# Kernel tuning notes

Hardware: AMD Instinct MI355X
Metric: run time of the kernel (lower is better)

Reference implementation:

```python
import jax, jax.numpy as jnp
import numpy as np

B, S, D, H = 4, 1024, 512, 8
DH = D // H  # dim_head = 64
LN_EPS = 1e-5
COS_EPS = 1e-8


def setup_inputs() -> dict:
    key = jax.random.key(0)
    ks = jax.random.split(key, 8)
    q = jax.random.normal(ks[0], (B, S, D), dtype=jnp.float32)
    k = jax.random.normal(ks[1], (B, S, D), dtype=jnp.float32)
    v = jax.random.normal(ks[2], (B, S, D), dtype=jnp.float32)
    ln_g = jnp.ones((D,), jnp.float32)
    ln_b = jnp.zeros((D,), jnp.float32)
    W_in = jax.random.normal(ks[3], (D, D), dtype=jnp.float32) / np.sqrt(D)
    W_out = jax.random.normal(ks[4], (D, D), dtype=jnp.float32) / np.sqrt(D)
    b_out = jnp.zeros((D,), jnp.float32)
    cov_w = jnp.float32(0.6)
    var_w = jnp.float32(0.2)
    return {"q": q, "k": k, "v": v, "ln_g": ln_g, "ln_b": ln_b,
            "W_in": W_in, "W_out": W_out, "b_out": b_out,
            "cov_w": cov_w, "var_w": var_w}


def reference(q, k, v, ln_g, ln_b, W_in, W_out, b_out, cov_w, var_w):
    def transform(x):
        # input_layernorm followed by bias-free input_linear
        mu = jnp.mean(x, axis=-1, keepdims=True)
        var = jnp.var(x, axis=-1, keepdims=True)
        xn = (x - mu) * jax.lax.rsqrt(var + LN_EPS) * ln_g + ln_b
        y = xn @ W_in
        # 'q n (h d) -> h q n d'
        return y.reshape(B, S, H, DH).transpose(2, 0, 1, 3)

    f_q = transform(q)  # [h, b, n, d]
    f_k = transform(k)  # [h, b, m, d]
    f_v = transform(v)  # [h, b, m, d]

    # cosine_distance(f_q, f_k^T)
    dots = jnp.einsum('hbnd,hbmd->hbnm', f_q, f_k)
    qn = jnp.linalg.norm(f_q, axis=-1)  # [h, b, n]
    kn = jnp.linalg.norm(f_k, axis=-1)  # [h, b, m]
    cosine_sim = dots / (qn[..., :, None] * kn[..., None, :] + COS_EPS)

    # basic_attention_components
    q_c = f_q - jnp.mean(f_q, axis=-1, keepdims=True)
    k_c = f_k - jnp.mean(f_k, axis=-1, keepdims=True)
    cov_component = jnp.einsum('hbnd,hbmd->hbnm', q_c, k_c) / DH
    q_var = jnp.var(f_q, axis=-1, ddof=1)  # torch.var unbiased=True
    k_var = jnp.var(f_k, axis=-1, ddof=1)
    var_component = (q_var[..., :, None] * k_var[..., None, :]) / DH

    # fixed learned-scalar mixing (dynamic_weight=False path)
    attn = (cov_w * cov_component + var_w * var_component
            + (1.0 - cov_w - var_w) * cosine_sim)

    out = jnp.einsum('hbnm,hbmd->hbnd', attn, f_v)
    # 'h q n d -> q n (h d)'
    out = out.transpose(1, 2, 0, 3).reshape(B, S, D)
    return out @ W_out + b_out
```

## Files before the change

### kernel.cpp

```cpp
#include <hip/hip_runtime.h>


#define R_TOT 4096
#define DD 512
#define HB_N 32

typedef __attribute__((ext_vector_type(8))) short short8;
typedef __attribute__((ext_vector_type(4))) float f32x4;

static __device__ inline unsigned short f2bf(float f) {
    union { float f; unsigned u; } x{f};
    unsigned r = x.u + 0x7fff + ((x.u >> 16) & 1);
    return (unsigned short)(r >> 16);
}

static __device__ inline unsigned scale2(unsigned u, float a, float b) {
    float lo = __uint_as_float(u << 16);
    float hi = __uint_as_float(u & 0xffff0000u);
    return (unsigned)f2bf(lo * a) | ((unsigned)f2bf(hi * b) << 16);
}

static __device__ inline void async_cp16(const unsigned short* g, unsigned short* l) {
    __builtin_amdgcn_global_load_lds(
        (const __attribute__((address_space(1))) unsigned int*)g,
        (__attribute__((address_space(3))) unsigned int*)l, 16, 0, 0);
}

__global__ __launch_bounds__(256) void k1_ln_prep(
    const float* __restrict__ q, const float* __restrict__ k, const float* __restrict__ v,
    const float* __restrict__ ln_g, const float* __restrict__ ln_b,
    const float* __restrict__ Win, const float* __restrict__ Wout,
    unsigned short* __restrict__ xn, unsigned short* __restrict__ WinT,
    unsigned short* __restrict__ WoutT)
{
    int blk = blockIdx.x;
    int t = threadIdx.x, lane = t & 63, wv = t >> 6;
    if (blk < 3072) {
        int row = blk * 4 + wv;
        const float* src = (row < R_TOT) ? q : (row < 2 * R_TOT ? k : v);
        const float* x = src + (size_t)(row & (R_TOT - 1)) * DD + lane * 8;
        float4 v0 = *(const float4*)x;
        float4 v1 = *(const float4*)(x + 4);
        float s  = v0.x + v0.y + v0.z + v0.w + v1.x + v1.y + v1.z + v1.w;
        float s2 = v0.x * v0.x + v0.y * v0.y + v0.z * v0.z + v0.w * v0.w
                 + v1.x * v1.x + v1.y * v1.y + v1.z * v1.z + v1.w * v1.w;
        #pragma unroll
        for (int o = 32; o; o >>= 1) { s += __shfl_xor(s, o); s2 += __shfl_xor(s2, o); }
        float mu = s * (1.f / 512.f);
        float var = s2 * (1.f / 512.f) - mu * mu;
        float rstd = rsqrtf(var + 1e-5f);
        float4 g0 = *(const float4*)(ln_g + lane * 8);
        float4 g1 = *(const float4*)(ln_g + lane * 8 + 4);
        float4 b0 = *(const float4*)(ln_b + lane * 8);
        float4 b1 = *(const float4*)(ln_b + lane * 8 + 4);
        float e0 = (v0.x - mu) * rstd * g0.x + b0.x;
        float e1 = (v0.y - mu) * rstd * g0.y + b0.y;
        float e2 = (v0.z - mu) * rstd * g0.z + b0.z;
        float e3 = (v0.w - mu) * rstd * g0.w + b0.w;
        float e4 = (v1.x - mu) * rstd * g1.x + b1.x;
        float e5 = (v1.y - mu) * rstd * g1.y + b1.y;
        float e6 = (v1.z - mu) * rstd * g1.z + b1.z;
        float e7 = (v1.w - mu) * rstd * g1.w + b1.w;
        uint4 o;
        o.x = (unsigned)f2bf(e0) | ((unsigned)f2bf(e1) << 16);
        o.y = (unsigned)f2bf(e2) | ((unsigned)f2bf(e3) << 16);
        o.z = (unsigned)f2bf(e4) | ((unsigned)f2bf(e5) << 16);
        o.w = (unsigned)f2bf(e6) | ((unsigned)f2bf(e7) << 16);
        *(uint4*)(xn + (size_t)row * DD + lane * 8) = o;
    } else {
        __shared__ float tl[64][65];
        int bb = blk - 3072;
        const float* src = (bb & 64) ? Wout : Win;
        unsigned short* dst = (bb & 64) ? WoutT : WinT;
        int tile = bb & 63;
        int r0 = (tile >> 3) * 64, c0 = (tile & 7) * 64;
        #pragma unroll
        for (int rep = 0; rep < 16; rep++) {
            int rr = rep * 4 + (t >> 6), cc = t & 63;
            tl[rr][cc] = src[(size_t)(r0 + rr) * DD + c0 + cc];
        }
        __syncthreads();
        #pragma unroll
        for (int rep = 0; rep < 16; rep++) {
            int rr = rep * 4 + (t >> 6), cc = t & 63;
            dst[(size_t)(c0 + rr) * DD + r0 + cc] = f2bf(tl[cc][rr]);
        }
    }
}

__global__ __launch_bounds__(256) void gemm_qkv(
    const unsigned short* __restrict__ A, const unsigned short* __restrict__ Bt,
    unsigned short* __restrict__ A2, unsigned short* __restrict__ Kt,
    unsigned short* __restrict__ Vt, float* __restrict__ kinv,
    float* __restrict__ kvar, float* __restrict__ kmu)
{
    __shared__ __align__(16) char smbuf[39936];
    unsigned short* AsF = (unsigned short*)smbuf;
    unsigned short* BsF = (unsigned short*)(smbuf + 16384);
    int t = threadIdx.x, lane = t & 63, wv = t >> 6;
    int quad = lane >> 4, l15 = lane & 15;
    int m0 = blockIdx.y * 128, n0 = blockIdx.x * 128;
    int wr = (wv >> 1) * 64, wc = (wv & 1) * 64;
    int swz = l15 & 7;
    int r8 = lane >> 3, cc8 = lane & 7;
    f32x4 acc[4][4] = {};
    for (int kt = 0; kt < 512; kt += 64) {
        __syncthreads();
        #pragma unroll
        for (int gi = 0; gi < 4; gi++) {
            int grp = wv * 4 + gi;
            int row = grp * 8 + r8;
            int col = kt + ((cc8 ^ (row & 7)) << 3);
            async_cp16(A + (size_t)(m0 + row) * 512 + col, AsF + grp * 512);
            async_cp16(Bt + (size_t)(n0 + row) * 512 + col, BsF + grp * 512);
        }
        __syncthreads();
        #pragma unroll
        for (int kk = 0; kk < 2; kk++) {
            short8 af[4], bf[4];
            int ksl = ((kk * 4 + quad) ^ swz) << 3;
            #pragma unroll
            for (int i = 0; i < 4; i++) af[i] = *(const short8*)&AsF[(wr + i * 16 + l15) * 64 + ksl];
            #pragma unroll
            for (int j = 0; j < 4; j++) bf[j] = *(const short8*)&BsF[(wc + j * 16 + l15) * 64 + ksl];
            #pragma unroll
            for (int i = 0; i < 4; i++)
                #pragma unroll
                for (int j = 0; j < 4; j++)
                    acc[i][j] = __builtin_amdgcn_mfma_f32_16x16x32_bf16(af[i], bf[j], acc[i][j], 0, 0, 0);
        }
    }
    __syncthreads();

    unsigned short* tile = (unsigned short*)(smbuf + wv * 9216);
    float* st     = (float*)(smbuf + 36864 + wv * 768);
    float* st_inv = st;
    float* st_var = st + 64;
    float* st_mu  = st + 128;

    int typ  = m0 >> 12;
    int rloc = (m0 & 4095) + wr;
    int b = rloc >> 10, sb = rloc & 1023;
    int h = (n0 + wc) >> 6;
    int hb = h * 4 + b;

    if (typ < 2) {
        #pragma unroll
        for (int i = 0; i < 4; i++)
            #pragma unroll
            for (int r = 0; r < 4; r++) {
                float a0 = acc[i][0][r], a1 = acc[i][1][r], a2 = acc[i][2][r], a3 = acc[i][3][r];
                float s1 = a0 + a1 + a2 + a3;
                float s2 = a0 * a0 + a1 * a1 + a2 * a2 + a3 * a3;
                #pragma unroll
                for (int o = 1; o < 16; o <<= 1) { s1 += __shfl_xor(s1, o); s2 += __shfl_xor(s2, o); }
                if (l15 == 0) {
                    int sl = i * 16 + quad * 4 + r;
                    float mu = s1 * (1.f / 64.f);
                    st_inv[sl] = rsqrtf(fmaxf(s2, 1e-20f));
                    st_var[sl] = (s2 - 64.f * mu * mu) * (1.f / 63.f);
                    st_mu[sl]  = mu;
                }
            }
    }
    #pragma unroll
    for (int i = 0; i < 4; i++)
        #pragma unroll
        for (int j = 0; j < 4; j++)
            #pragma unroll
            for (int r = 0; r < 4; r++) {
                int sl = i * 16 + quad * 4 + r, d = j * 16 + l15;
                unsigned short bv = f2bf(acc[i][j][r]);
                tile[(typ == 0) ? (sl * 72 + d) : (d * 72 + sl)] = bv;
            }

    if (typ == 0) {
        unsigned short* ob = A2 + ((size_t)hb * 1024 + sb) * 160;
        #pragma unroll
        for (int it = 0; it < 8; it++) {
            int sl = it * 8 + (lane >> 3), ch = (lane & 7) * 8;
            uint4 raw = *(uint4*)&tile[sl * 72 + ch];
            *(uint4*)(ob + (size_t)sl * 160 + ch) = raw;
            float iv = st_inv[sl];
            uint4 o2;
            o2.x = scale2(raw.x, iv, iv); o2.y = scale2(raw.y, iv, iv);
            o2.z = scale2(raw.z, iv, iv); o2.w = scale2(raw.w, iv, iv);
            *(uint4*)(ob + (size_t)sl * 160 + 64 + ch) = o2;
        }
        {
            int sl = lane;
            uint4 z = {0, 0, 0, 0};
            uint4 t0 = z;
            t0.x = (unsigned)f2bf(st_var[sl]) | ((unsigned)f2bf(st_mu[sl]) << 16);
            unsigned short* p = ob + (size_t)sl * 160 + 128;
            *(uint4*)p = t0;
            *(uint4*)(p + 8) = z; *(uint4*)(p + 16) = z; *(uint4*)(p + 24) = z;
        }
    } else if (typ == 1) {
        unsigned short* kb = Kt + (size_t)hb * 64 * 1024 + sb;
        #pragma unroll
        for (int it = 0; it < 8; it++) {
            int d = it * 8 + (lane >> 3), ch = (lane & 7) * 8;
            uint4 raw = *(uint4*)&tile[d * 72 + ch];
            *(uint4*)(kb + (size_t)d * 1024 + ch) = raw;
        }
        int mi = hb * 1024 + sb + lane;
        kinv[mi] = st_inv[lane];
        kvar[mi] = st_var[lane];
        kmu[mi]  = st_mu[lane];
    } else {
        unsigned short* vb = Vt + (size_t)hb * 64 * 1024 + sb;
        #pragma unroll
        for (int it = 0; it < 8; it++) {
            int d = it * 8 + (lane >> 3), ch = (lane & 7) * 8;
            uint4 raw = *(uint4*)&tile[d * 72 + ch];
            *(uint4*)(vb + (size_t)d * 1024 + ch) = raw;
        }
    }
}

__global__ __launch_bounds__(256) void k45_ktv(
    const unsigned short* __restrict__ Kt, const unsigned short* __restrict__ Vt,
    const float* __restrict__ kinv, const float* __restrict__ kvar,
    const float* __restrict__ kmu, unsigned short* __restrict__ B2t,
    const float* __restrict__ covp, const float* __restrict__ varp)
{
    __shared__ __align__(16) unsigned short As[144][136];
    __shared__ __align__(16) unsigned short Bs[64][136];
    __shared__ float sinv[128], svar[128], smu[128];
    int hb = blockIdx.x;
    int t = threadIdx.x, lane = t & 63, wv = t >> 6;
    int quad = lane >> 4, l15 = lane & 15;
    float cov = covp[0], vw = varp[0];
    float c1 = cov * (1.f / 64.f), cw = 1.f - cov - vw;
    float vw64 = vw * (1.f / 64.f), c2 = -cov;
    const unsigned short* Kb = Kt + (size_t)hb * 64 * 1024;
    const unsigned short* Vb = Vt + (size_t)hb * 64 * 1024;
    int sbase = hb * 1024;
    if (t < 224) {
        int row = 130 + (t >> 4), co = (t & 15) * 8;
        uint4 z = {0, 0, 0, 0};
        *(uint4*)&As[row][co] = z;
    }
    f32x4 acc[9] = {};
    for (int kc = 0; kc < 8; kc++) {
        __syncthreads();
        if (t < 128) {
            int m = kc * 128 + t;
            sinv[t] = kinv[sbase + m]; svar[t] = kvar[sbase + m]; smu[t] = kmu[sbase + m];
        }
        uint4 kraw[4];
        #pragma unroll
        for (int i = 0; i < 4; i++) {
            int id = i * 256 + t, row = id >> 4, co = (id & 15) * 8;
            kraw[i] = *(const uint4*)(Kb + (size_t)row * 1024 + kc * 128 + co);
            *(uint4*)&As[row][co] = kraw[i];
            uint4 vr = *(const uint4*)(Vb + (size_t)row * 1024 + kc * 128 + co);
            *(uint4*)&Bs[row][co] = vr;
        }
        __syncthreads();
        #pragma unroll
        for (int i = 0; i < 4; i++) {
            int id = i * 256 + t, row = id >> 4, co = (id & 15) * 8;
            float4 iva = *(const float4*)&sinv[co];
            float4 ivb = *(const float4*)&sinv[co + 4];
            uint4 o;
            o.x = scale2(kraw[i].x, iva.x, iva.y); o.y = scale2(kraw[i].y, iva.z, iva.w);
            o.z = scale2(kraw[i].z, ivb.x, ivb.y); o.w = scale2(kraw[i].w, ivb.z, ivb.w);
            *(uint4*)&As[64 + row][co] = o;
        }
        if (t < 32) {
            int which = t >> 4, j0 = (t & 15) * 8;
            const float* sp = (which ? smu : svar) + j0;
            uint4 o;
            o.x = (unsigned)f2bf(sp[0]) | ((unsigned)f2bf(sp[1]) << 16);
            o.y = (unsigned)f2bf(sp[2]) | ((unsigned)f2bf(sp[3]) << 16);
            o.z = (unsigned)f2bf(sp[4]) | ((unsigned)f2bf(sp[5]) << 16);
            o.w = (unsigned)f2bf(sp[6]) | ((unsigned)f2bf(sp[7]) << 16);
            *(uint4*)&As[128 + which][j0] = o;
        }
        __syncthreads();
        #pragma unroll
        for (int kk = 0; kk < 4; kk++) {
            short8 bfrag = *(const short8*)&Bs[wv * 16 + l15][kk * 32 + quad * 8];
            #pragma unroll
            for (int mt = 0; mt < 9; mt++) {
                short8 afrag = *(const short8*)&As[mt * 16 + l15][kk * 32 + quad * 8];
                acc[mt] = __builtin_amdgcn_mfma_f32_16x16x32_bf16(afrag, bfrag, acc[mt], 0, 0, 0);
            }
        }
    }
    unsigned short* ob = B2t + (size_t)hb * 10240;
    int d = wv * 16 + l15;
    #pragma unroll
    for (int mt = 0; mt < 9; mt++)
        #pragma unroll
        for (int r = 0; r < 4; r++) {
            int kk = mt * 16 + quad * 4 + r;
            float scale = (kk < 64) ? c1 : (kk < 128) ? cw : (kk == 128) ? vw64 : (kk == 129) ? c2 : 0.f;
            ob[d * 160 + kk] = f2bf(scale * acc[mt][r]);
        }
}

__global__ __launch_bounds__(256) void k6_apply(
    const unsigned short* __restrict__ A2, const unsigned short* __restrict__ B2t,
    unsigned short* __restrict__ g)
{
    int hb = blockIdx.y, h = hb >> 2, b = hb & 3;
    int m0 = blockIdx.x * 128;
    int t = threadIdx.x, lane = t & 63, wv = t >> 6;
    int quad = lane >> 4, l15 = lane & 15;
    __shared__ __align__(16) unsigned short As[128][40];
    __shared__ __align__(16) unsigned short Bs[64][40];
    const unsigned short* Ab = A2 + (size_t)hb * 1024 * 160;
    const unsigned short* Bb = B2t + (size_t)hb * 10240;
    f32x4 acc[2][4] = {};
    for (int kt = 0; kt < 160; kt += 32) {
        __syncthreads();
        #pragma unroll
        for (int ld = 0; ld < 2; ld++) {
            int id = ld * 256 + t;
            int row = id >> 2, co = (id & 3) * 8;
            *(uint4*)&As[row][co] = *(const uint4*)(Ab + (size_t)(m0 + row) * 160 + kt + co);
        }
        {
            int row = t >> 2, co = (t & 3) * 8;
            *(uint4*)&Bs[row][co] = *(const uint4*)(Bb + (size_t)row * 160 + kt + co);
        }
        __syncthreads();
        short8 af[2], bf[4];
        #pragma unroll
        for (int i = 0; i < 2; i++) af[i] = *(const short8*)&As[wv * 32 + i * 16 + l15][quad * 8];
        #pragma unroll
        for (int j = 0; j < 4; j++) bf[j] = *(const short8*)&Bs[j * 16 + l15][quad * 8];
        #pragma unroll
        for (int i = 0; i < 2; i++)
            #pragma unroll
            for (int j = 0; j < 4; j++)
                acc[i][j] = __builtin_amdgcn_mfma_f32_16x16x32_bf16(af[i], bf[j], acc[i][j], 0, 0, 0);
    }
    #pragma unroll
    for (int i = 0; i < 2; i++)
        #pragma unroll
        for (int j = 0; j < 4; j++)
            #pragma unroll
            for (int r = 0; r < 4; r++) {
                int rr = m0 + wv * 32 + i * 16 + quad * 4 + r;
                int cc = j * 16 + l15;
                g[((size_t)b * 1024 + rr) * 512 + h * 64 + cc] = f2bf(acc[i][j][r]);
            }
}

__global__ __launch_bounds__(256) void gemm_out(
    const unsigned short* __restrict__ A, const unsigned short* __restrict__ Bt,
    float* __restrict__ C, const float* __restrict__ bias)
{
    __shared__ __align__(16) unsigned short As[128][40];
    __shared__ __align__(16) unsigned short Bs[64][40];
    int t = threadIdx.x, lane = t & 63, wv = t >> 6;
    int quad = lane >> 4, l15 = lane & 15;
    int m0 = blockIdx.y * 128, n0 = blockIdx.x * 64;
    f32x4 acc[2][4] = {};
    for (int kt = 0; kt < 512; kt += 32) {
        __syncthreads();
        #pragma unroll
        for (int ld = 0; ld < 2; ld++) {
            int id = ld * 256 + t;
            int row = id >> 2, co = (id & 3) * 8;
            *(uint4*)&As[row][co] = *(const uint4*)(A + (size_t)(m0 + row) * 512 + kt + co);
        }
        {
            int row = t >> 2, co = (t & 3) * 8;
            *(uint4*)&Bs[row][co] = *(const uint4*)(Bt + (size_t)(n0 + row) * 512 + kt + co);
        }
        __syncthreads();
        short8 af[2], bf[4];
        #pragma unroll
        for (int i = 0; i < 2; i++) af[i] = *(const short8*)&As[wv * 32 + i * 16 + l15][quad * 8];
        #pragma unroll
        for (int j = 0; j < 4; j++) bf[j] = *(const short8*)&Bs[j * 16 + l15][quad * 8];
        #pragma unroll
        for (int i = 0; i < 2; i++)
            #pragma unroll
            for (int j = 0; j < 4; j++)
                acc[i][j] = __builtin_amdgcn_mfma_f32_16x16x32_bf16(af[i], bf[j], acc[i][j], 0, 0, 0);
    }
    #pragma unroll
    for (int i = 0; i < 2; i++)
        #pragma unroll
        for (int j = 0; j < 4; j++)
            #pragma unroll
            for (int r = 0; r < 4; r++) {
                int rr = m0 + wv * 32 + i * 16 + quad * 4 + r;
                int cc = n0 + j * 16 + l15;
                C[(size_t)rr * 512 + cc] = acc[i][j][r] + bias[cc];
            }
}

extern "C" void kernel_launch(void* const* d_in, const int* in_sizes, int n_in,
                              void* d_out, int out_size, void* d_ws, size_t ws_size,
                              hipStream_t stream)
{
    const float* q    = (const float*)d_in[0];
    const float* k    = (const float*)d_in[1];
    const float* v    = (const float*)d_in[2];
    const float* ln_g = (const float*)d_in[3];
    const float* ln_b = (const float*)d_in[4];
    const float* Win  = (const float*)d_in[5];
    const float* Wout = (const float*)d_in[6];
    const float* bout = (const float*)d_in[7];
    const float* covw = (const float*)d_in[8];
    const float* varw = (const float*)d_in[9];

    char* ws = (char*)d_ws;
    size_t off = 0;
    auto alloc = [&](size_t bytes) { size_t r = off; off += (bytes + 255) & ~(size_t)255; return r; };
    unsigned short* xn    = (unsigned short*)(ws + alloc((size_t)3 * R_TOT * DD * 2));
    unsigned short* WinT  = (unsigned short*)(ws + alloc((size_t)DD * DD * 2));
    unsigned short* WoutT = (unsigned short*)(ws + alloc((size_t)DD * DD * 2));
    unsigned short* A2    = (unsigned short*)(ws + alloc((size_t)HB_N * 1024 * 160 * 2));
    unsigned short* Kt    = (unsigned short*)(ws + alloc((size_t)HB_N * 64 * 1024 * 2));
    unsigned short* Vt    = (unsigned short*)(ws + alloc((size_t)HB_N * 64 * 1024 * 2));
    float*          kinv  = (float*)(ws + alloc((size_t)HB_N * 1024 * 4));
    float*          kvar  = (float*)(ws + alloc((size_t)HB_N * 1024 * 4));
    float*          kmu   = (float*)(ws + alloc((size_t)HB_N * 1024 * 4));
    unsigned short* g     = (unsigned short*)(ws + alloc((size_t)R_TOT * DD * 2));
    unsigned short* B2t   = (unsigned short*)(ws + alloc((size_t)HB_N * 10240 * 2));
    (void)ws_size; (void)in_sizes; (void)n_in; (void)out_size;

    k1_ln_prep<<<3072 + 128, 256, 0, stream>>>(q, k, v, ln_g, ln_b, Win, Wout, xn, WinT, WoutT);
    gemm_qkv<<<dim3(4, 96), 256, 0, stream>>>(xn, WinT, A2, Kt, Vt, kinv, kvar, kmu);
    k45_ktv<<<HB_N, 256, 0, stream>>>(Kt, Vt, kinv, kvar, kmu, B2t, covw, varw);
    k6_apply<<<dim3(8, HB_N), 256, 0, stream>>>(A2, B2t, g);
    gemm_out<<<dim3(8, 32), 256, 0, stream>>>(g, WoutT, (float*)d_out, bout);
}
```

Before: 148.4 us.

## Fold output projection into per-head K^T V matrix and fuse apply with output GEMM

Per head/batch, the small (160x64) K^T V combination matrix is now multiplied by the head's slice of W_out inside k45_ktv, giving a 160x512 matrix per head-batch. A single k6_out kernel then contracts A2 across all heads against these folded matrices and writes the final fp32 output with bias. This drops the intermediate g buffer and one kernel launch. In exchange the apply GEMM has K=8*160=1280 instead of 512, and k45_ktv does extra serial work over only 32 blocks.

```diff
diff --git a/kernel.cpp b/kernel.cpp
--- a/kernel.cpp
+++ b/kernel.cpp
@@ -222,7 +222,8 @@
 __global__ __launch_bounds__(256) void k45_ktv(
     const unsigned short* __restrict__ Kt, const unsigned short* __restrict__ Vt,
     const float* __restrict__ kinv, const float* __restrict__ kvar,
-    const float* __restrict__ kmu, unsigned short* __restrict__ B2t,
+    const float* __restrict__ kmu, const unsigned short* __restrict__ WoutT,
+    unsigned short* __restrict__ Rbuf,
     const float* __restrict__ covp, const float* __restrict__ varp)
 {
     __shared__ __align__(16) unsigned short As[144][136];
@@ -290,54 +291,86 @@
             }
         }
     }
-    unsigned short* ob = B2t + (size_t)hb * 10240;
-    int d = wv * 16 + l15;
-    #pragma unroll
-    for (int mt = 0; mt < 9; mt++)
-        #pragma unroll
-        for (int r = 0; r < 4; r++) {
-            int kk = mt * 16 + quad * 4 + r;
-            float scale = (kk < 64) ? c1 : (kk < 128) ? cw : (kk == 128) ? vw64 : (kk == 129) ? c2 : 0.f;
-            ob[d * 160 + kk] = f2bf(scale * acc[mt][r]);
-        }
-}
-
-__global__ __launch_bounds__(256) void k6_apply(
-    const unsigned short* __restrict__ A2, const unsigned short* __restrict__ B2t,
-    unsigned short* __restrict__ g)
+    __syncthreads();
+    unsigned short* Ls = (unsigned short*)As;
+    {
+        int d = wv * 16 + l15;
+        #pragma unroll
+        for (int mt = 0; mt < 9; mt++)
+            #pragma unroll
+            for (int r = 0; r < 4; r++) {
+                int kk = mt * 16 + quad * 4 + r;
+                float scale = (kk < 64) ? c1 : (kk < 128) ? cw : (kk == 128) ? vw64 : (kk == 129) ? c2 : 0.f;
+                Ls[kk * 72 + d] = f2bf(scale * acc[mt][r]);
+            }
+        #pragma unroll
+        for (int r = 0; r < 4; r++)
+            Ls[(144 + quad * 4 + r) * 72 + d] = 0;
+    }
+    __syncthreads();
+    int h = hb >> 2;
+    unsigned short* Rb = Rbuf + (size_t)hb * 8 * 64 * 160;
+    for (int nt = 0; nt < 8; nt++) {
+        int n = nt * 64 + wv * 16 + l15;
+        f32x4 a2[10] = {};
+        #pragma unroll
+        for (int kk2 = 0; kk2 < 2; kk2++) {
+            short8 bfrag = *(const short8*)(WoutT + (size_t)n * 512 + h * 64 + kk2 * 32 + quad * 8);
+            #pragma unroll
+            for (int mt = 0; mt < 10; mt++) {
+                short8 afrag = *(const short8*)&Ls[(mt * 16 + l15) * 72 + kk2 * 32 + quad * 8];
+                a2[mt] = __builtin_amdgcn_mfma_f32_16x16x32_bf16(afrag, bfrag, a2[mt], 0, 0, 0);
+            }
+        }
+        unsigned short* ro = Rb + ((size_t)nt * 64 + wv * 16 + l15) * 160;
+        #pragma unroll
+        for (int mt = 0; mt < 10; mt++)
+            #pragma unroll
+            for (int r = 0; r < 4; r++)
+                ro[mt * 16 + quad * 4 + r] = f2bf(a2[mt][r]);
+    }
+}
+
+__global__ __launch_bounds__(256) void k6_out(
+    const unsigned short* __restrict__ A2, const unsigned short* __restrict__ Rbuf,
+    float* __restrict__ C, const float* __restrict__ bias)
 {
-    int hb = blockIdx.y, h = hb >> 2, b = hb & 3;
-    int m0 = blockIdx.x * 128;
+    int m0 = blockIdx.y * 128;
+    int nt = blockIdx.x;
+    int b = m0 >> 10, s0 = m0 & 1023;
     int t = threadIdx.x, lane = t & 63, wv = t >> 6;
     int quad = lane >> 4, l15 = lane & 15;
     __shared__ __align__(16) unsigned short As[128][40];
     __shared__ __align__(16) unsigned short Bs[64][40];
-    const unsigned short* Ab = A2 + (size_t)hb * 1024 * 160;
-    const unsigned short* Bb = B2t + (size_t)hb * 10240;
     f32x4 acc[2][4] = {};
-    for (int kt = 0; kt < 160; kt += 32) {
-        __syncthreads();
-        #pragma unroll
-        for (int ld = 0; ld < 2; ld++) {
-            int id = ld * 256 + t;
-            int row = id >> 2, co = (id & 3) * 8;
-            *(uint4*)&As[row][co] = *(const uint4*)(Ab + (size_t)(m0 + row) * 160 + kt + co);
-        }
-        {
-            int row = t >> 2, co = (t & 3) * 8;
-            *(uint4*)&Bs[row][co] = *(const uint4*)(Bb + (size_t)row * 160 + kt + co);
-        }
-        __syncthreads();
-        short8 af[2], bf[4];
-        #pragma unroll
-        for (int i = 0; i < 2; i++) af[i] = *(const short8*)&As[wv * 32 + i * 16 + l15][quad * 8];
-        #pragma unroll
-        for (int j = 0; j < 4; j++) bf[j] = *(const short8*)&Bs[j * 16 + l15][quad * 8];
-        #pragma unroll
-        for (int i = 0; i < 2; i++)
-            #pragma unroll
-            for (int j = 0; j < 4; j++)
-                acc[i][j] = __builtin_amdgcn_mfma_f32_16x16x32_bf16(af[i], bf[j], acc[i][j], 0, 0, 0);
+    for (int h = 0; h < 8; h++) {
+        int hb = h * 4 + b;
+        const unsigned short* Ab = A2 + ((size_t)hb * 1024 + s0) * 160;
+        const unsigned short* Bb = Rbuf + ((size_t)(hb * 8 + nt)) * 64 * 160;
+        for (int kt = 0; kt < 160; kt += 32) {
+            __syncthreads();
+            #pragma unroll
+            for (int ld = 0; ld < 2; ld++) {
+                int id = ld * 256 + t;
+                int row = id >> 2, co = (id & 3) * 8;
+                *(uint4*)&As[row][co] = *(const uint4*)(Ab + (size_t)row * 160 + kt + co);
+            }
+            {
+                int row = t >> 2, co = (t & 3) * 8;
+                *(uint4*)&Bs[row][co] = *(const uint4*)(Bb + (size_t)row * 160 + kt + co);
+            }
+            __syncthreads();
+            short8 af[2], bf[4];
+            #pragma unroll
+            for (int i = 0; i < 2; i++) af[i] = *(const short8*)&As[wv * 32 + i * 16 + l15][quad * 8];
+            #pragma unroll
+            for (int j = 0; j < 4; j++) bf[j] = *(const short8*)&Bs[j * 16 + l15][quad * 8];
+            #pragma unroll
+            for (int i = 0; i < 2; i++)
+                #pragma unroll
+                for (int j = 0; j < 4; j++)
+                    acc[i][j] = __builtin_amdgcn_mfma_f32_16x16x32_bf16(af[i], bf[j], acc[i][j], 0, 0, 0);
+        }
     }
     #pragma unroll
     for (int i = 0; i < 2; i++)
@@ -346,53 +379,7 @@
             #pragma unroll
             for (int r = 0; r < 4; r++) {
                 int rr = m0 + wv * 32 + i * 16 + quad * 4 + r;
-                int cc = j * 16 + l15;
-                g[((size_t)b * 1024 + rr) * 512 + h * 64 + cc] = f2bf(acc[i][j][r]);
-            }
-}
-
-__global__ __launch_bounds__(256) void gemm_out(
-    const unsigned short* __restrict__ A, const unsigned short* __restrict__ Bt,
-    float* __restrict__ C, const float* __restrict__ bias)
-{
-    __shared__ __align__(16) unsigned short As[128][40];
-    __shared__ __align__(16) unsigned short Bs[64][40];
-    int t = threadIdx.x, lane = t & 63, wv = t >> 6;
-    int quad = lane >> 4, l15 = lane & 15;
-    int m0 = blockIdx.y * 128, n0 = blockIdx.x * 64;
-    f32x4 acc[2][4] = {};
-    for (int kt = 0; kt < 512; kt += 32) {
-        __syncthreads();
-        #pragma unroll
-        for (int ld = 0; ld < 2; ld++) {
-            int id = ld * 256 + t;
-            int row = id >> 2, co = (id & 3) * 8;
-            *(uint4*)&As[row][co] = *(const uint4*)(A + (size_t)(m0 + row) * 512 + kt + co);
-        }
-        {
-            int row = t >> 2, co = (t & 3) * 8;
-            *(uint4*)&Bs[row][co] = *(const uint4*)(Bt + (size_t)(n0 + row) * 512 + kt + co);
-        }
-        __syncthreads();
-        short8 af[2], bf[4];
-        #pragma unroll
-        for (int i = 0; i < 2; i++) af[i] = *(const short8*)&As[wv * 32 + i * 16 + l15][quad * 8];
-        #pragma unroll
-        for (int j = 0; j < 4; j++) bf[j] = *(const short8*)&Bs[j * 16 + l15][quad * 8];
-        #pragma unroll
-        for (int i = 0; i < 2; i++)
-            #pragma unroll
-            for (int j = 0; j < 4; j++)
-                acc[i][j] = __builtin_amdgcn_mfma_f32_16x16x32_bf16(af[i], bf[j], acc[i][j], 0, 0, 0);
-    }
-    #pragma unroll
-    for (int i = 0; i < 2; i++)
-        #pragma unroll
-        for (int j = 0; j < 4; j++)
-            #pragma unroll
-            for (int r = 0; r < 4; r++) {
-                int rr = m0 + wv * 32 + i * 16 + quad * 4 + r;
-                int cc = n0 + j * 16 + l15;
+                int cc = nt * 64 + j * 16 + l15;
                 C[(size_t)rr * 512 + cc] = acc[i][j][r] + bias[cc];
             }
 }
@@ -424,13 +411,11 @@
     float*          kinv  = (float*)(ws + alloc((size_t)HB_N * 1024 * 4));
     float*          kvar  = (float*)(ws + alloc((size_t)HB_N * 1024 * 4));
     float*          kmu   = (float*)(ws + alloc((size_t)HB_N * 1024 * 4));
-    unsigned short* g     = (unsigned short*)(ws + alloc((size_t)R_TOT * DD * 2));
-    unsigned short* B2t   = (unsigned short*)(ws + alloc((size_t)HB_N * 10240 * 2));
+    unsigned short* Rbuf  = (unsigned short*)(ws + alloc((size_t)HB_N * 8 * 64 * 160 * 2));
     (void)ws_size; (void)in_sizes; (void)n_in; (void)out_size;
 
     k1_ln_prep<<<3072 + 128, 256, 0, stream>>>(q, k, v, ln_g, ln_b, Win, Wout, xn, WinT, WoutT);
     gemm_qkv<<<dim3(4, 96), 256, 0, stream>>>(xn, WinT, A2, Kt, Vt, kinv, kvar, kmu);
-    k45_ktv<<<HB_N, 256, 0, stream>>>(Kt, Vt, kinv, kvar, kmu, B2t, covw, varw);
-    k6_apply<<<dim3(8, HB_N), 256, 0, stream>>>(A2, B2t, g);
-    gemm_out<<<dim3(8, 32), 256, 0, stream>>>(g, WoutT, (float*)d_out, bout);
-}
+    k45_ktv<<<HB_N, 256, 0, stream>>>(Kt, Vt, kinv, kvar, kmu, WoutT, Rbuf, covw, varw);
+    k6_out<<<dim3(8, 32), 256, 0, stream>>>(A2, Rbuf, (float*)d_out, bout);
+}
```

After: 163.7 us. 1.1x slower.
